# Optimization experiments

Measured on AMD Instinct MI355X. Metric: run time of the kernel, lower is better.

The kernel has to match this reference:

```python
import math
import jax, jax.numpy as jnp
import numpy as np

# config (matches env defaults of the torch module, scaled to production size)
V, D, L, NH, NKV, MLP_M, RECUR, N_VB = 32768, 1024, 6, 16, 8, 3, 2, 5
BG_BK, BG_DIM = 4096, 128
HD = D // NH            # 64 head dim
KV = NKV * HD           # 512 kv width
B, T = 2, 1024
SOFTCAP = 30.0
EPS = 1.1920929e-07     # fp32 eps used by F.rms_norm(eps=None)


def _rms(x):
    return x * jax.lax.rsqrt(jnp.mean(jnp.square(x), axis=-1, keepdims=True) + EPS)


def _rope(x, c, s):
    h = x.shape[-1] // 2
    x1, x2 = x[..., :h], x[..., h:]
    return jnp.concatenate([x1 * c + x2 * s, -x1 * s + x2 * c], axis=-1)


def _forward(ids, tgt, emb, bg_embed, bg_proj, bg_scale, ve,
             Wq, Wk, Wv, Wo, qg, a_s, m_s, mix, Wfc, Wpr):
    Bz, Tz = ids.shape
    # token embedding + bigram-hash embedding
    x = emb[ids]
    t = ids.astype(jnp.int32)
    hv = jnp.bitwise_xor(t[:, 1:] * 36313, t[:, :-1] * 27191) % (BG_BK - 1)
    h = jnp.zeros_like(t).at[:, 1:].set(hv)
    bg = (bg_embed[h] @ bg_proj) * bg_scale
    x = _rms(x + bg)
    x0 = x
    # rope tables
    inv = 1.0 / (10000.0 ** (jnp.arange(0, HD, 2, dtype=jnp.float32) / HD))
    ang = jnp.arange(Tz, dtype=jnp.float32)[:, None] * inv      # (T, HD/2)
    c, s = jnp.cos(ang)[None, None], jnp.sin(ang)[None, None]   # (1,1,T,HD/2)
    mask = jnp.tril(jnp.ones((Tz, Tz), dtype=bool))
    eff = 0
    for _ in range(RECUR):
        for l in range(L):
            vel = ve[eff % N_VB][ids]                            # (B,T,KV)
            m = mix[l]
            x = m[0] * x + m[1] * x0
            # attention
            xn = _rms(x)
            q = (xn @ Wq[l]).reshape(Bz, Tz, NH, HD).transpose(0, 2, 1, 3)
            k = (xn @ Wk[l]).reshape(Bz, Tz, NKV, HD).transpose(0, 2, 1, 3)
            v = ((xn @ Wv[l]) + vel).reshape(Bz, Tz, NKV, HD).transpose(0, 2, 1, 3)
            q, k = _rms(q), _rms(k)
            q, k = _rope(q, c, s), _rope(k, c, s)
            q = q * qg[l][None, :, None, None]
            rep = NH // NKV                                      # GQA expand
            kf = jnp.repeat(k, rep, axis=1)
            vf = jnp.repeat(v, rep, axis=1)
            sc = jnp.einsum('bhqd,bhkd->bhqk', q, kf) / math.sqrt(HD)
            sc = jnp.where(mask, sc, -jnp.inf)
            att = jax.nn.softmax(sc, axis=-1)
            y = jnp.einsum('bhqk,bhkd->bhqd', att, vf)
            y = y.transpose(0, 2, 1, 3).reshape(Bz, Tz, D) @ Wo[l]
            x = x + a_s[l] * y
            # mlp: relu(fc(x))^2 @ proj
            hmid = jnp.square(jax.nn.relu(_rms(x) @ Wfc[l]))
            x = x + m_s[l] * (hmid @ Wpr[l])
            eff += 1
    x = _rms(x)
    lo = x @ emb.T
    lo = SOFTCAP * jnp.tanh(lo / SOFTCAP)
    logp = jax.nn.log_softmax(lo, axis=-1)
    nll = -jnp.take_along_axis(logp, tgt[..., None], axis=-1)[..., 0]
    return jnp.mean(nll)


def setup_inputs() -> dict:
    key = jax.random.key(0)
    ks = jax.random.split(key, 14)
    def nrm(k, shape, std):
        return std * jax.random.normal(k, shape, dtype=jnp.float32)
    eff = L * RECUR
    return {
        'ids': jax.random.randint(ks[0], (B, T), 0, V),
        'tgt': jax.random.randint(ks[1], (B, T), 0, V),
        'emb': nrm(ks[2], (V, D), 0.005),
        'bg_embed': nrm(ks[3], (BG_BK, BG_DIM), 0.02),
        'bg_proj': nrm(ks[4], (BG_DIM, D), 1.0 / math.sqrt(BG_DIM)),
        'bg_scale': jnp.float32(0.05),
        've': nrm(ks[5], (N_VB, V, KV), 0.01),
        'Wq': nrm(ks[6], (L, D, D), 1.0 / math.sqrt(D)),
        'Wk': nrm(ks[7], (L, D, KV), 1.0 / math.sqrt(D)),
        'Wv': nrm(ks[8], (L, D, KV), 1.0 / math.sqrt(D)),
        'Wo': nrm(ks[9], (L, D, D), 1.0 / (math.sqrt(D) * math.sqrt(2 * eff))),
        'qg': jnp.full((L, NH), 1.5, jnp.float32),
        'a_s': jnp.ones((L, D), jnp.float32),
        'm_s': jnp.ones((L, D), jnp.float32),
        'mix': jnp.stack([jnp.ones((L, D)), jnp.zeros((L, D))], axis=1).astype(jnp.float32),
        'Wfc': nrm(ks[10], (L, D, MLP_M * D), 1.0 / math.sqrt(D)),
        'Wpr': nrm(ks[11], (L, MLP_M * D, D), 1.0 / (math.sqrt(MLP_M * D) * math.sqrt(2 * eff))),
    }


def reference(ids, tgt, emb, bg_embed, bg_proj, bg_scale, ve,
              Wq, Wk, Wv, Wo, qg, a_s, m_s, mix, Wfc, Wpr):
    return _forward(ids, tgt, emb, bg_embed, bg_proj, bg_scale, ve,
                    Wq, Wk, Wv, Wo, qg, a_s, m_s, mix, Wfc, Wpr)
```

## Files before the change

### kernel.cpp

```cpp
#include <hip/hip_runtime.h>
#include <hip/hip_bf16.h>
#include <math.h>

#define DEV __device__ __forceinline__

typedef unsigned short u16;
typedef short bf16x8 __attribute__((ext_vector_type(8)));
typedef float f32x4 __attribute__((ext_vector_type(4)));
typedef u16 u16x8 __attribute__((ext_vector_type(8)));
typedef u16 u16x4 __attribute__((ext_vector_type(4)));

#define T_SEQ 1024
#define NTOK 2048
#define DIM 1024
#define NHD 16
#define NKVH 8
#define HDIM 64
#define KVD 512
#define MLPD 3072
#define VOC 32768
#define EPSF 1.1920929e-07f
#define SCAP 30.0f
#define NCB 512
#define PSTRIDE ((size_t)NTOK * DIM)

#define MEMFENCE asm volatile("" ::: "memory")

DEV u16 f2b(float f) {
  __hip_bfloat16 h = __float2bfloat16(f);
  u16 r; __builtin_memcpy(&r, &h, 2); return r;
}
DEV float b2f(u16 u) {
  __hip_bfloat16 h; __builtin_memcpy(&h, &u, 2);
  return __bfloat162float(h);
}

DEV void gload16(const void* g, void* l) {
  __builtin_amdgcn_global_load_lds((const __attribute__((address_space(1))) void*)g,
                                   (__attribute__((address_space(3))) void*)l, 16, 0, 0);
}

DEV float blk_sum256(float v, float* sbuf) {
#pragma unroll
  for (int o = 32; o; o >>= 1) v += __shfl_xor(v, o, 64);
  int w = threadIdx.x >> 6;
  if ((threadIdx.x & 63) == 0) sbuf[w] = v;
  __syncthreads();
  return sbuf[0] + sbuf[1] + sbuf[2] + sbuf[3];
}

__global__ __launch_bounds__(256) void transpose_f2b(const float* __restrict__ in,
    u16* __restrict__ out, int K, int N, size_t in_ls, size_t out_ls) {
  __shared__ float tile[32][33];
  int l = blockIdx.z;
  const float* src = in + (size_t)l * in_ls;
  u16* dst = out + (size_t)l * out_ls;
  int k0 = blockIdx.y << 5, n0 = blockIdx.x << 5;
  int tx = threadIdx.x & 31, ty = threadIdx.x >> 5;
#pragma unroll
  for (int i = 0; i < 32; i += 8)
    tile[ty + i][tx] = src[(size_t)(k0 + ty + i) * N + n0 + tx];
  __syncthreads();
#pragma unroll
  for (int i = 0; i < 32; i += 8)
    dst[(size_t)(n0 + ty + i) * K + k0 + tx] = f2b(tile[tx][ty + i]);
}

__global__ __launch_bounds__(256) void f2b_copy(const float* __restrict__ in,
    u16* __restrict__ out, size_t n) {
  size_t i = ((size_t)blockIdx.x * 256 + threadIdx.x) * 8;
  if (i >= n) return;
  float4 a = *(const float4*)(in + i);
  float4 b = *(const float4*)(in + i + 4);
  u16x8 o;
  o[0] = f2b(a.x); o[1] = f2b(a.y); o[2] = f2b(a.z); o[3] = f2b(a.w);
  o[4] = f2b(b.x); o[5] = f2b(b.y); o[6] = f2b(b.z); o[7] = f2b(b.w);
  *(u16x8*)(out + i) = o;
}

__global__ __launch_bounds__(256) void rope_table(float* __restrict__ rc, float* __restrict__ rs) {
  int idx = blockIdx.x * 256 + threadIdx.x;
  if (idx >= T_SEQ * 32) return;
  int t = idx >> 5, i = idx & 31;
  float inv = expf(-((float)(2 * i) / (float)HDIM) * logf(10000.0f));
  float ang = (float)t * inv;
  rc[idx] = cosf(ang);
  rs[idx] = sinf(ang);
}

__global__ __launch_bounds__(256) void embed_kernel(const int* __restrict__ ids,
    const float* __restrict__ emb, const float* __restrict__ bg_embed,
    const float* __restrict__ bg_proj, const float* __restrict__ bg_scale_p,
    float* __restrict__ x, float* __restrict__ x0) {
  __shared__ float be[128];
  __shared__ float sbuf[4];
  int tok = blockIdx.x, tid = threadIdx.x;
  int t = tok & (T_SEQ - 1);
  int id = ids[tok];
  int hsh = 0;
  if (t > 0) {
    int prev = ids[tok - 1];
    hsh = ((id * 36313) ^ (prev * 27191)) % 4095;
  }
  if (tid < 128) be[tid] = bg_embed[hsh * 128 + tid];
  __syncthreads();
  float scale = bg_scale_p[0];
  const float4* bp = (const float4*)bg_proj;
  float ax = 0.f, ay = 0.f, az = 0.f, aw = 0.f;
#pragma unroll 4
  for (int j = 0; j < 128; ++j) {
    float bj = be[j];
    float4 p = bp[j * 256 + tid];
    ax += bj * p.x; ay += bj * p.y; az += bj * p.z; aw += bj * p.w;
  }
  float4 e = *(const float4*)(emb + (size_t)id * DIM + tid * 4);
  float vx = e.x + ax * scale, vy = e.y + ay * scale;
  float vz = e.z + az * scale, vw = e.w + aw * scale;
  float ss = vx * vx + vy * vy + vz * vz + vw * vw;
  float tot = blk_sum256(ss, sbuf);
  float rn = rsqrtf(tot * (1.0f / DIM) + EPSF);
  float4 o; o.x = vx * rn; o.y = vy * rn; o.z = vz * rn; o.w = vw * rn;
  size_t base = (size_t)tok * DIM + tid * 4;
  *(float4*)(x + base) = o;
  *(float4*)(x0 + base) = o;
}

template <int NP, int MIX>
__global__ __launch_bounds__(256) void norm_k(float* __restrict__ x,
    const float* __restrict__ parts, const float* __restrict__ colscale,
    const float* __restrict__ mixl, const float* __restrict__ x0,
    u16* __restrict__ xn) {
  __shared__ float sbuf[4];
  int tok = blockIdx.x, tid = threadIdx.x;
  size_t base = (size_t)tok * DIM + tid * 4;
  float4 a = *(const float4*)(x + base);
  if (NP > 0) {
    float4 cs = *(const float4*)(colscale + tid * 4);
    float4 s = *(const float4*)(parts + base);
    {
      float4 p = *(const float4*)(parts + PSTRIDE + base);
      s.x += p.x; s.y += p.y; s.z += p.z; s.w += p.w;
    }
    if (NP == 3) {
      float4 p = *(const float4*)(parts + 2 * PSTRIDE + base);
      s.x += p.x; s.y += p.y; s.z += p.z; s.w += p.w;
    }
    a.x += cs.x * s.x; a.y += cs.y * s.y; a.z += cs.z * s.z; a.w += cs.w * s.w;
  }
  if (MIX) {
    float4 m0 = *(const float4*)(mixl + tid * 4);
    float4 m1 = *(const float4*)(mixl + DIM + tid * 4);
    float4 b = *(const float4*)(x0 + base);
    a.x = m0.x * a.x + m1.x * b.x;
    a.y = m0.y * a.y + m1.y * b.y;
    a.z = m0.z * a.z + m1.z * b.z;
    a.w = m0.w * a.w + m1.w * b.w;
  }
  float ss = a.x * a.x + a.y * a.y + a.z * a.z + a.w * a.w;
  float tot = blk_sum256(ss, sbuf);
  float rn = rsqrtf(tot * (1.0f / DIM) + EPSF);
  if (NP > 0 || MIX) *(float4*)(x + base) = a;
  u16x4 q;
  q[0] = f2b(a.x * rn); q[1] = f2b(a.y * rn); q[2] = f2b(a.z * rn); q[3] = f2b(a.w * rn);
  *(u16x4*)(xn + base) = q;
}

template <int EPI, int BN>
__global__ __launch_bounds__(256, (BN == 64 ? 3 : 2)) void gemm_bt(
    const u16* __restrict__ A, const u16* __restrict__ Bt,
    float* __restrict__ Cf, u16* __restrict__ Cb,
    int N, int K, int kpn) {
  constexpr int MF = (BN == 128) ? 4 : 2;
  constexpr int ASZ = 128 * 64;
  constexpr int BSZ = BN * 64;
  constexpr int NLD = 4 + BN / 32;
  __shared__ u16 As[2 * ASZ];
  __shared__ u16 Bs[2 * BSZ];
  int tid = threadIdx.x;
  int wid = tid >> 6, lane = tid & 63;
  int g = lane >> 4, c = lane & 15;
  int row0 = blockIdx.y << 7, col0 = blockIdx.x * BN;
  int kbase = blockIdx.z * kpn;
  int wr = (BN == 128) ? ((wid >> 1) << 6) : (wid << 5);
  int wc = (BN == 128) ? ((wid & 1) << 6) : 0;
  f32x4 acc[MF][4] = {};

  int sr = lane >> 3;
  int kb = lane & 7;
  const u16* srcA[4];
  int ldsA[4];
#pragma unroll
  for (int i = 0; i < 4; ++i) {
    int s = (wid << 2) + i;
    int r = (s << 3) + sr;
    srcA[i] = A + (size_t)(row0 + r) * K + kbase + ((kb ^ (r & 7)) << 3);
    ldsA[i] = s << 9;
  }
  const u16* srcB[BN / 32];
  int ldsB[BN / 32];
#pragma unroll
  for (int i = 0; i < BN / 32; ++i) {
    int s = wid * (BN / 32) + i;
    int r = (s << 3) + sr;
    srcB[i] = Bt + (size_t)(col0 + r) * K + kbase + ((kb ^ (r & 7)) << 3);
    ldsB[i] = s << 9;
  }

#pragma unroll
  for (int i = 0; i < 4; ++i) gload16(srcA[i], As + ldsA[i]);
#pragma unroll
  for (int i = 0; i < BN / 32; ++i) gload16(srcB[i], Bs + ldsB[i]);

  int nk = kpn >> 6;
  for (int t = 0; t < nk; ++t) {
    int cur = t & 1;
    if (t + 1 < nk) {
      int nxt = cur ^ 1;
      int ko = (t + 1) << 6;
#pragma unroll
      for (int i = 0; i < 4; ++i) gload16(srcA[i] + ko, As + nxt * ASZ + ldsA[i]);
#pragma unroll
      for (int i = 0; i < BN / 32; ++i) gload16(srcB[i] + ko, Bs + nxt * BSZ + ldsB[i]);
      if constexpr (NLD == 6) asm volatile("s_waitcnt vmcnt(6)" ::: "memory");
      else asm volatile("s_waitcnt vmcnt(8)" ::: "memory");
    } else {
      asm volatile("s_waitcnt vmcnt(0)" ::: "memory");
    }
    __builtin_amdgcn_s_barrier();
    MEMFENCE;
    const u16* ab = As + cur * ASZ;
    const u16* bb = Bs + cur * BSZ;
#pragma unroll
    for (int ks = 0; ks < 2; ++ks) {
      bf16x8 af[MF], bfr[4];
#pragma unroll
      for (int m = 0; m < MF; ++m) {
        int r = wr + m * 16 + c;
        int kbs = ((ks << 2) + g) ^ (r & 7);
        af[m] = *(const bf16x8*)(ab + r * 64 + (kbs << 3));
      }
#pragma unroll
      for (int n = 0; n < 4; ++n) {
        int r = wc + n * 16 + c;
        int kbs = ((ks << 2) + g) ^ (r & 7);
        bfr[n] = *(const bf16x8*)(bb + r * 64 + (kbs << 3));
      }
      __builtin_amdgcn_s_setprio(1);
#pragma unroll
      for (int m = 0; m < MF; ++m)
#pragma unroll
        for (int n = 0; n < 4; ++n)
          acc[m][n] = __builtin_amdgcn_mfma_f32_16x16x32_bf16(af[m], bfr[n], acc[m][n], 0, 0, 0);
      __builtin_amdgcn_s_setprio(0);
    }
    MEMFENCE;
    __builtin_amdgcn_s_barrier();
  }

  size_t zoff = (size_t)blockIdx.z * PSTRIDE;
#pragma unroll
  for (int m = 0; m < MF; ++m) {
#pragma unroll
    for (int n = 0; n < 4; ++n) {
      int gcol = col0 + wc + n * 16 + c;
#pragma unroll
      for (int j = 0; j < 4; ++j) {
        int grow = row0 + wr + m * 16 + g * 4 + j;
        float v = acc[m][n][j];
        if (EPI == 1) {
          Cf[zoff + (size_t)grow * N + gcol] = v;
        } else if (EPI == 2) {
          float r = v > 0.f ? v : 0.f;
          Cb[(size_t)grow * N + gcol] = f2b(r * r);
        }
      }
    }
  }
}

__global__ __launch_bounds__(512, 2) void gemm_lmhead(
    const u16* __restrict__ A, const u16* __restrict__ Bt,
    const int* __restrict__ tgt, float* __restrict__ pM, float* __restrict__ pS,
    float* __restrict__ loTgt) {
  constexpr int K = 1024;
  constexpr int TSZ = 256 * 64;
  __shared__ u16 As[2 * TSZ];
  __shared__ u16 Bs[2 * TSZ];
  int tid = threadIdx.x;
  int wid = tid >> 6, lane = tid & 63;
  int wm = wid >> 2, wn = wid & 3;
  int g = lane >> 4, c = lane & 15;
  int bid = blockIdx.x;
  int swz = ((bid & 7) << 7) + (bid >> 3);
  int colb = swz >> 3, rowb = swz & 7;
  int row0 = rowb << 8, col0 = colb << 8;
  f32x4 acc[8][4] = {};

  int sr = lane >> 3, kb = lane & 7;
  const u16* srcA[4];
  const u16* srcB[4];
  int ldsOff[4];
#pragma unroll
  for (int i = 0; i < 4; ++i) {
    int s = (wid << 2) + i;
    int r = (s << 3) + sr;
    srcA[i] = A + (size_t)(row0 + r) * K + ((kb ^ (r & 7)) << 3);
    srcB[i] = Bt + (size_t)(col0 + r) * K + ((kb ^ (r & 7)) << 3);
    ldsOff[i] = s << 9;
  }

#pragma unroll
  for (int i = 0; i < 4; ++i) {
    gload16(srcA[i], As + ldsOff[i]);
    gload16(srcB[i], Bs + ldsOff[i]);
  }

  constexpr int nk = K >> 6;
  for (int kt = 0; kt < nk; ++kt) {
    int cur = kt & 1;
    if (kt + 1 < nk) {
      int nxt = cur ^ 1;
      int ko = (kt + 1) << 6;
#pragma unroll
      for (int i = 0; i < 4; ++i) {
        gload16(srcA[i] + ko, As + nxt * TSZ + ldsOff[i]);
        gload16(srcB[i] + ko, Bs + nxt * TSZ + ldsOff[i]);
      }
      asm volatile("s_waitcnt vmcnt(8)" ::: "memory");
    } else {
      asm volatile("s_waitcnt vmcnt(0)" ::: "memory");
    }
    __builtin_amdgcn_s_barrier();
    MEMFENCE;
    const u16* ab = As + cur * TSZ;
    const u16* bb = Bs + cur * TSZ;
    bf16x8 bfr[4][2];
#pragma unroll
    for (int nf = 0; nf < 4; ++nf) {
      int r = (wn << 6) + nf * 16 + c;
#pragma unroll
      for (int ks = 0; ks < 2; ++ks) {
        int kbs = ((ks << 2) + g) ^ (r & 7);
        bfr[nf][ks] = *(const bf16x8*)(bb + r * 64 + (kbs << 3));
      }
    }
#pragma unroll
    for (int p = 0; p < 4; ++p) {
      bf16x8 af[2][2];
#pragma unroll
      for (int mi = 0; mi < 2; ++mi) {
        int r = (wm << 7) + ((p << 1) + mi) * 16 + c;
#pragma unroll
        for (int ks = 0; ks < 2; ++ks) {
          int kbs = ((ks << 2) + g) ^ (r & 7);
          af[mi][ks] = *(const bf16x8*)(ab + r * 64 + (kbs << 3));
        }
      }
      __builtin_amdgcn_s_setprio(1);
#pragma unroll
      for (int ks = 0; ks < 2; ++ks)
#pragma unroll
        for (int mi = 0; mi < 2; ++mi)
#pragma unroll
          for (int nf = 0; nf < 4; ++nf)
            acc[(p << 1) + mi][nf] = __builtin_amdgcn_mfma_f32_16x16x32_bf16(
                af[mi][ks], bfr[nf][ks], acc[(p << 1) + mi][nf], 0, 0, 0);
      __builtin_amdgcn_s_setprio(0);
    }
    MEMFENCE;
    __builtin_amdgcn_s_barrier();
  }

  int cb = (col0 >> 6) + wn;
#pragma unroll
  for (int mf = 0; mf < 8; ++mf) {
#pragma unroll
    for (int j = 0; j < 4; ++j) {
      int grow = row0 + (wm << 7) + mf * 16 + g * 4 + j;
      int tg = tgt[grow];
      float sv[4];
      float mx = -3.0e38f;
#pragma unroll
      for (int nf = 0; nf < 4; ++nf) {
        float a = acc[mf][nf][j] * (1.0f / SCAP);
        a = fminf(fmaxf(a, -15.f), 15.f);
        float e = __expf(2.0f * a);
        float tt = SCAP * (e - 1.0f) / (e + 1.0f);
        sv[nf] = tt;
        mx = fmaxf(mx, tt);
        int gcol = col0 + (wn << 6) + nf * 16 + c;
        if (gcol == tg) loTgt[grow] = tt;
      }
      mx = fmaxf(mx, __shfl_xor(mx, 1, 64));
      mx = fmaxf(mx, __shfl_xor(mx, 2, 64));
      mx = fmaxf(mx, __shfl_xor(mx, 4, 64));
      mx = fmaxf(mx, __shfl_xor(mx, 8, 64));
      float s = 0.f;
#pragma unroll
      for (int nf = 0; nf < 4; ++nf) s += __expf(sv[nf] - mx);
      s += __shfl_xor(s, 1, 64);
      s += __shfl_xor(s, 2, 64);
      s += __shfl_xor(s, 4, 64);
      s += __shfl_xor(s, 8, 64);
      if (c == 0) {
        pM[(size_t)grow * NCB + cb] = mx;
        pS[(size_t)grow * NCB + cb] = s;
      }
    }
  }
}

__global__ __launch_bounds__(256, 3) void gemm_qkv(
    const u16* __restrict__ A, const u16* __restrict__ Bt,
    const float* __restrict__ qg_l, const float* __restrict__ rc, const float* __restrict__ rs,
    const float* __restrict__ ve, const int* __restrict__ ids, int vb,
    u16* __restrict__ qB, u16* __restrict__ kB, u16* __restrict__ vT) {
  constexpr int K = 1024;
  constexpr int ASZ = 128 * 64;
  constexpr int BSZ = 64 * 64;
  __shared__ u16 As[2 * ASZ];
  __shared__ u16 Bs[2 * BSZ];
  int tid = threadIdx.x;
  int wid = tid >> 6, lane = tid & 63;
  int g = lane >> 4, c = lane & 15;
  int bx = blockIdx.x;
  int row0 = blockIdx.y << 7, col0 = bx << 6;
  f32x4 acc[2][4] = {};

  int sr = lane >> 3, kb = lane & 7;
  const u16* srcA[4];
  int ldsA[4];
#pragma unroll
  for (int i = 0; i < 4; ++i) {
    int s = (wid << 2) + i;
    int r = (s << 3) + sr;
    srcA[i] = A + (size_t)(row0 + r) * K + ((kb ^ (r & 7)) << 3);
    ldsA[i] = s << 9;
  }
  const u16* srcB[2];
  int ldsB[2];
#pragma unroll
  for (int i = 0; i < 2; ++i) {
    int s = (wid << 1) + i;
    int r = (s << 3) + sr;
    srcB[i] = Bt + (size_t)(col0 + r) * K + ((kb ^ (r & 7)) << 3);
    ldsB[i] = s << 9;
  }

#pragma unroll
  for (int i = 0; i < 4; ++i) gload16(srcA[i], As + ldsA[i]);
#pragma unroll
  for (int i = 0; i < 2; ++i) gload16(srcB[i], Bs + ldsB[i]);

  for (int t = 0; t < 16; ++t) {
    int cur = t & 1;
    if (t + 1 < 16) {
      int nxt = cur ^ 1;
      int ko = (t + 1) << 6;
#pragma unroll
      for (int i = 0; i < 4; ++i) gload16(srcA[i] + ko, As + nxt * ASZ + ldsA[i]);
#pragma unroll
      for (int i = 0; i < 2; ++i) gload16(srcB[i] + ko, Bs + nxt * BSZ + ldsB[i]);
      asm volatile("s_waitcnt vmcnt(6)" ::: "memory");
    } else {
      asm volatile("s_waitcnt vmcnt(0)" ::: "memory");
    }
    __builtin_amdgcn_s_barrier();
    MEMFENCE;
    const u16* ab = As + cur * ASZ;
    const u16* bb = Bs + cur * BSZ;
#pragma unroll
    for (int ks = 0; ks < 2; ++ks) {
      bf16x8 af[2], bfr[4];
#pragma unroll
      for (int m = 0; m < 2; ++m) {
        int r = (wid << 5) + m * 16 + c;
        int kbs = ((ks << 2) + g) ^ (r & 7);
        af[m] = *(const bf16x8*)(ab + r * 64 + (kbs << 3));
      }
#pragma unroll
      for (int n = 0; n < 4; ++n) {
        int r = n * 16 + c;
        int kbs = ((ks << 2) + g) ^ (r & 7);
        bfr[n] = *(const bf16x8*)(bb + r * 64 + (kbs << 3));
      }
      __builtin_amdgcn_s_setprio(1);
#pragma unroll
      for (int m = 0; m < 2; ++m)
#pragma unroll
        for (int n = 0; n < 4; ++n)
          acc[m][n] = __builtin_amdgcn_mfma_f32_16x16x32_bf16(af[m], bfr[n], acc[m][n], 0, 0, 0);
      __builtin_amdgcn_s_setprio(0);
    }
    MEMFENCE;
    __builtin_amdgcn_s_barrier();
  }

  int b = row0 >> 10;
  if (bx < 24) {
    bool isq = (bx < 16);
    int h = isq ? bx : bx - 16;
    float gmul = isq ? qg_l[h] * 0.125f : 1.0f;
    u16* hb = isq ? (qB + ((size_t)(b * NHD + h)) * T_SEQ * HDIM)
                  : (kB + ((size_t)(b * NKVH + h)) * T_SEQ * HDIM);
#pragma unroll
    for (int m = 0; m < 2; ++m) {
#pragma unroll
      for (int j = 0; j < 4; ++j) {
        int grow = row0 + (wid << 5) + m * 16 + g * 4 + j;
        int t = grow & (T_SEQ - 1);
        float vv[4];
        float ss = 0.f;
#pragma unroll
        for (int n = 0; n < 4; ++n) { vv[n] = acc[m][n][j]; ss += vv[n] * vv[n]; }
        ss += __shfl_xor(ss, 1, 64);
        ss += __shfl_xor(ss, 2, 64);
        ss += __shfl_xor(ss, 4, 64);
        ss += __shfl_xor(ss, 8, 64);
        float rn = rsqrtf(ss * (1.0f / HDIM) + EPSF);
#pragma unroll
        for (int n = 0; n < 4; ++n) vv[n] *= rn;
        float c0 = rc[t * 32 + c], s0 = rs[t * 32 + c];
        float c1 = rc[t * 32 + 16 + c], s1 = rs[t * 32 + 16 + c];
        float o0 = vv[0] * c0 + vv[2] * s0;
        float o1 = vv[1] * c1 + vv[3] * s1;
        float o2 = vv[2] * c0 - vv[0] * s0;
        float o3 = vv[3] * c1 - vv[1] * s1;
        u16* dst = hb + (size_t)t * HDIM;
        dst[c] = f2b(o0 * gmul);
        dst[16 + c] = f2b(o1 * gmul);
        dst[32 + c] = f2b(o2 * gmul);
        dst[48 + c] = f2b(o3 * gmul);
      }
    }
  } else {
    int kh = bx - 24;
#pragma unroll
    for (int m = 0; m < 2; ++m) {
#pragma unroll
      for (int j = 0; j < 4; ++j) {
        int grow = row0 + (wid << 5) + m * 16 + g * 4 + j;
        int lr = (wid << 5) + m * 16 + g * 4 + j;
        int id = ids[grow];
        const float* vl = ve + ((size_t)vb * VOC + id) * KVD + kh * HDIM;
#pragma unroll
        for (int n = 0; n < 4; ++n)
          As[lr * 72 + n * 16 + c] = f2b(acc[m][n][j] + vl[n * 16 + c]);
      }
    }
    __syncthreads();
    int hd = tid & 63, seg = tid >> 6;
    int t0 = (row0 & (T_SEQ - 1)) + seg * 32;
    u16* dst = vT + (((size_t)(b * NKVH + kh)) * HDIM + hd) * T_SEQ + t0;
#pragma unroll
    for (int i = 0; i < 32; i += 8) {
      u16x8 o;
#pragma unroll
      for (int e = 0; e < 8; ++e) o[e] = As[(seg * 32 + i + e) * 72 + hd];
      *(u16x8*)(dst + i) = o;
    }
  }
}

__global__ __launch_bounds__(128) void attn_kernel(const u16* __restrict__ qB,
    const u16* __restrict__ kB, const u16* __restrict__ vT, const float* __restrict__ qg_l,
    u16* __restrict__ attout) {
  __shared__ u16 plds[2][32 * 76];
  int b = blockIdx.z, h = blockIdx.y;
  int kh = h >> 1;
  int wid = threadIdx.x >> 6, lane = threadIdx.x & 63;
  int g = lane >> 4, c = lane & 15;
  int strip = wid ? (31 - (int)blockIdx.x) : (int)blockIdx.x;
  int qr0 = strip << 5;
  const u16* qptr = qB + ((size_t)(b * NHD + h)) * T_SEQ * HDIM;
  const u16* kptr = kB + ((size_t)(b * NKVH + kh)) * T_SEQ * HDIM;
  const u16* vptr = vT + ((size_t)(b * NKVH + kh)) * HDIM * T_SEQ;
  u16* pw = plds[wid];
  float Mh = fabsf(qg_l[h]) * 8.0f;

  bf16x8 aq[2][2];
#pragma unroll
  for (int m = 0; m < 2; ++m)
#pragma unroll
    for (int ks = 0; ks < 2; ++ks)
      aq[m][ks] = *(const bf16x8*)(qptr + (qr0 + m * 16 + c) * HDIM + ks * 32 + g * 8);

  bf16x8 vone;
#pragma unroll
  for (int e = 0; e < 8; ++e) vone[e] = (short)0x3F80;

  f32x4 oacc[2][4] = {};
  f32x4 lacc[2] = {};

  bf16x8 kR0[4][2], vR0[4][2], kR1[4][2], vR1[4][2];

  auto LOADKV = [&](bf16x8 (&bk)[4][2], bf16x8 (&bv)[4][2], int kv0) {
#pragma unroll
    for (int n = 0; n < 4; ++n)
#pragma unroll
      for (int ks = 0; ks < 2; ++ks) {
        bk[n][ks] = *(const bf16x8*)(kptr + (kv0 + n * 16 + c) * HDIM + ks * 32 + g * 8);
        bv[n][ks] = *(const bf16x8*)(vptr + (n * 16 + c) * T_SEQ + kv0 + ks * 32 + g * 8);
      }
  };

  auto BODY = [&](bf16x8 (&bk)[4][2], bf16x8 (&bv)[4][2], int kv0) {
    f32x4 sc[2][4] = {};
#pragma unroll
    for (int ks = 0; ks < 2; ++ks)
#pragma unroll
      for (int m = 0; m < 2; ++m)
#pragma unroll
        for (int n = 0; n < 4; ++n)
          sc[m][n] = __builtin_amdgcn_mfma_f32_16x16x32_bf16(aq[m][ks], bk[n][ks], sc[m][n], 0, 0, 0);
    bool maskT = (kv0 + 64 > qr0);
#pragma unroll
    for (int m = 0; m < 2; ++m) {
#pragma unroll
      for (int j = 0; j < 4; ++j) {
        int row = qr0 + m * 16 + g * 4 + j;
        float p0 = __expf(sc[m][0][j] - Mh);
        float p1 = __expf(sc[m][1][j] - Mh);
        float p2 = __expf(sc[m][2][j] - Mh);
        float p3 = __expf(sc[m][3][j] - Mh);
        if (maskT) {
          if (kv0 + c > row) p0 = 0.f;
          if (kv0 + 16 + c > row) p1 = 0.f;
          if (kv0 + 32 + c > row) p2 = 0.f;
          if (kv0 + 48 + c > row) p3 = 0.f;
        }
        int pr = m * 16 + g * 4 + j;
        pw[pr * 76 + c] = f2b(p0);
        pw[pr * 76 + 16 + c] = f2b(p1);
        pw[pr * 76 + 32 + c] = f2b(p2);
        pw[pr * 76 + 48 + c] = f2b(p3);
      }
    }
    MEMFENCE;
    bf16x8 ap[2][2];
#pragma unroll
    for (int m = 0; m < 2; ++m)
#pragma unroll
      for (int ks = 0; ks < 2; ++ks) {
        u16x8 tmp = *(const u16x8*)(pw + (m * 16 + c) * 76 + ks * 32 + g * 8);
        __builtin_memcpy(&ap[m][ks], &tmp, 16);
      }
#pragma unroll
    for (int ks = 0; ks < 2; ++ks) {
#pragma unroll
      for (int m = 0; m < 2; ++m) {
#pragma unroll
        for (int n = 0; n < 4; ++n)
          oacc[m][n] = __builtin_amdgcn_mfma_f32_16x16x32_bf16(ap[m][ks], bv[n][ks], oacc[m][n], 0, 0, 0);
        lacc[m] = __builtin_amdgcn_mfma_f32_16x16x32_bf16(ap[m][ks], vone, lacc[m], 0, 0, 0);
      }
    }
  };

  LOADKV(kR0, vR0, 0);
  int kv0 = 0;
  while (true) {
    if (kv0 + 64 <= qr0) LOADKV(kR1, vR1, kv0 + 64);
    BODY(kR0, vR0, kv0);
    kv0 += 64;
    if (kv0 > qr0) break;
    if (kv0 + 64 <= qr0) LOADKV(kR0, vR0, kv0 + 64);
    BODY(kR1, vR1, kv0);
    kv0 += 64;
    if (kv0 > qr0) break;
  }

#pragma unroll
  for (int m = 0; m < 2; ++m) {
#pragma unroll
    for (int j = 0; j < 4; ++j) {
      float inv = 1.0f / lacc[m][j];
      int trow = qr0 + m * 16 + g * 4 + j;
      u16* orow = attout + ((size_t)(b * T_SEQ + trow)) * DIM + h * HDIM;
#pragma unroll
      for (int n = 0; n < 4; ++n)
        orow[n * 16 + c] = f2b(oacc[m][n][j] * inv);
    }
  }
}

__global__ __launch_bounds__(256) void lse_merge(const float* __restrict__ pM,
    const float* __restrict__ pS, const float* __restrict__ loTgt, float* __restrict__ nll) {
  __shared__ float sbuf[4];
  int tok = blockIdx.x, tid = threadIdx.x;
  int wid = tid >> 6, lane = tid & 63;
  const float* rm = pM + (size_t)tok * NCB;
  const float* rs = pS + (size_t)tok * NCB;
  float m0 = rm[tid], m1 = rm[tid + 256];
  float mx = fmaxf(m0, m1);
#pragma unroll
  for (int o = 32; o; o >>= 1) mx = fmaxf(mx, __shfl_xor(mx, o, 64));
  if (lane == 0) sbuf[wid] = mx;
  __syncthreads();
  float M = fmaxf(fmaxf(sbuf[0], sbuf[1]), fmaxf(sbuf[2], sbuf[3]));
  __syncthreads();
  float s = rs[tid] * __expf(m0 - M) + rs[tid + 256] * __expf(m1 - M);
  float S = blk_sum256(s, sbuf);
  if (tid == 0) nll[tok] = logf(S) + M - loTgt[tok];
}

__global__ __launch_bounds__(256) void loss_final(const float* __restrict__ nll,
    float* __restrict__ out) {
  __shared__ float sbuf[4];
  int tid = threadIdx.x;
  float acc = 0.f;
  for (int i = tid; i < NTOK; i += 256) acc += nll[i];
  float tot = blk_sum256(acc, sbuf);
  if (tid == 0) out[0] = tot * (1.0f / NTOK);
}

extern "C" void kernel_launch(void* const* d_in, const int* in_sizes, int n_in,
                              void* d_out, int out_size, void* d_ws, size_t ws_size,
                              hipStream_t stream) {
  (void)in_sizes; (void)n_in; (void)out_size; (void)ws_size;
  const int* ids = (const int*)d_in[0];
  const int* tgt = (const int*)d_in[1];
  const float* emb = (const float*)d_in[2];
  const float* bg_embed = (const float*)d_in[3];
  const float* bg_proj = (const float*)d_in[4];
  const float* bg_scale = (const float*)d_in[5];
  const float* ve = (const float*)d_in[6];
  const float* Wq = (const float*)d_in[7];
  const float* Wk = (const float*)d_in[8];
  const float* Wv = (const float*)d_in[9];
  const float* Wo = (const float*)d_in[10];
  const float* qg = (const float*)d_in[11];
  const float* a_s = (const float*)d_in[12];
  const float* m_s = (const float*)d_in[13];
  const float* mix = (const float*)d_in[14];
  const float* Wfc = (const float*)d_in[15];
  const float* Wpr = (const float*)d_in[16];

  char* w = (char*)d_ws;
  auto alloc = [&](size_t bytes) {
    char* p = w;
    w += (bytes + 255) & ~(size_t)255;
    return p;
  };
  u16* WqkvT = (u16*)alloc(6ull * 2048 * 1024 * 2);
  u16* WoT   = (u16*)alloc(6ull * 1024 * 1024 * 2);
  u16* WfcT  = (u16*)alloc(6ull * 3072 * 1024 * 2);
  u16* WprT  = (u16*)alloc(6ull * 1024 * 3072 * 2);
  u16* embB  = (u16*)alloc((size_t)VOC * DIM * 2);
  float* x   = (float*)alloc((size_t)NTOK * DIM * 4);
  float* x0  = (float*)alloc((size_t)NTOK * DIM * 4);
  u16* xn    = (u16*)alloc((size_t)NTOK * DIM * 2);
  u16* qBuf  = (u16*)alloc((size_t)NTOK * DIM * 2);
  u16* kBuf  = (u16*)alloc((size_t)NTOK * KVD * 2);
  u16* vTb   = (u16*)alloc((size_t)NTOK * KVD * 2);
  u16* attout = (u16*)alloc((size_t)NTOK * DIM * 2);
  u16* xmlp  = (u16*)alloc((size_t)NTOK * DIM * 2);
  u16* hmid  = (u16*)alloc((size_t)NTOK * MLPD * 2);
  float* pparts = (float*)alloc(3 * PSTRIDE * 4);
  float* rc  = (float*)alloc((size_t)T_SEQ * 32 * 4);
  float* rs  = (float*)alloc((size_t)T_SEQ * 32 * 4);
  float* pM  = (float*)alloc((size_t)NTOK * NCB * 4);
  float* pS  = (float*)alloc((size_t)NTOK * NCB * 4);
  float* loTgt = (float*)alloc(NTOK * 4);
  float* nll = (float*)alloc(NTOK * 4);

  transpose_f2b<<<dim3(32, 32, 6), 256, 0, stream>>>(Wq, WqkvT, 1024, 1024,
      (size_t)1024 * 1024, (size_t)2048 * 1024);
  transpose_f2b<<<dim3(16, 32, 6), 256, 0, stream>>>(Wk, WqkvT + 1024 * 1024, 1024, 512,
      (size_t)1024 * 512, (size_t)2048 * 1024);
  transpose_f2b<<<dim3(16, 32, 6), 256, 0, stream>>>(Wv, WqkvT + 1536 * 1024, 1024, 512,
      (size_t)1024 * 512, (size_t)2048 * 1024);
  transpose_f2b<<<dim3(32, 32, 6), 256, 0, stream>>>(Wo, WoT, 1024, 1024,
      (size_t)1024 * 1024, (size_t)1024 * 1024);
  transpose_f2b<<<dim3(96, 32, 6), 256, 0, stream>>>(Wfc, WfcT, 1024, 3072,
      (size_t)1024 * 3072, (size_t)3072 * 1024);
  transpose_f2b<<<dim3(32, 96, 6), 256, 0, stream>>>(Wpr, WprT, 3072, 1024,
      (size_t)3072 * 1024, (size_t)1024 * 3072);
  f2b_copy<<<16384, 256, 0, stream>>>(emb, embB, (size_t)VOC * DIM);
  rope_table<<<128, 256, 0, stream>>>(rc, rs);
  embed_kernel<<<NTOK, 256, 0, stream>>>(ids, emb, bg_embed, bg_proj, bg_scale, x, x0);

  int lprev = 0;
  for (int step = 0; step < 12; ++step) {
    int l = step % 6;
    if (step == 0)
      norm_k<0, 1><<<NTOK, 256, 0, stream>>>(x, nullptr, nullptr, mix + l * 2048, x0, xn);
    else
      norm_k<3, 1><<<NTOK, 256, 0, stream>>>(x, pparts, m_s + lprev * DIM, mix + l * 2048, x0, xn);
    gemm_qkv<<<dim3(32, 16), 256, 0, stream>>>(xn, WqkvT + (size_t)l * 2048 * 1024,
        qg + l * 16, rc, rs, ve, ids, step % 5, qBuf, kBuf, vTb);
    attn_kernel<<<dim3(16, 16, 2), 128, 0, stream>>>(qBuf, kBuf, vTb, qg + l * 16, attout);
    gemm_bt<1, 64><<<dim3(16, 16, 2), 256, 0, stream>>>(attout, WoT + (size_t)l * 1024 * 1024,
        pparts, nullptr, 1024, 1024, 512);
    norm_k<2, 0><<<NTOK, 256, 0, stream>>>(x, pparts, a_s + l * DIM, nullptr, nullptr, xmlp);
    gemm_bt<2, 64><<<dim3(48, 16, 1), 256, 0, stream>>>(xmlp, WfcT + (size_t)l * 3072 * 1024,
        nullptr, hmid, 3072, 1024, 1024);
    gemm_bt<1, 64><<<dim3(16, 16, 3), 256, 0, stream>>>(hmid, WprT + (size_t)l * 1024 * 3072,
        pparts, nullptr, 1024, 3072, 1024);
    lprev = l;
  }

  norm_k<3, 0><<<NTOK, 256, 0, stream>>>(x, pparts, m_s + lprev * DIM, nullptr, nullptr, xn);
  gemm_lmhead<<<1024, 512, 0, stream>>>(xn, embB, tgt, pM, pS, loTgt);
  lse_merge<<<NTOK, 256, 0, stream>>>(pM, pS, loTgt, nll);
  loss_final<<<1, 256, 0, stream>>>(nll, (float*)d_out);
}
```

Before: 1.868 ms.

## Split attention KV range across two blocks and merge partials; fuse prep kernels

Attention is split along the KV dimension: each block handles every other 64-wide KV tile. The two blocks write unnormalized fp32 partial outputs and row sums, and a new merge kernel adds them and normalizes into bf16. This doubles the attention grid to fill more compute units, since the old grid had only 512 blocks of 128 threads. In exchange it adds an fp32 round trip through global memory and one extra launch per layer. The weight-transpose, embedding-conversion and rope-table setup kernels are also merged into one launch to cut launch overhead.

```diff
diff --git a/kernel.cpp b/kernel.cpp
--- a/kernel.cpp
+++ b/kernel.cpp
@@ -49,43 +49,56 @@
   return sbuf[0] + sbuf[1] + sbuf[2] + sbuf[3];
 }
 
-__global__ __launch_bounds__(256) void transpose_f2b(const float* __restrict__ in,
-    u16* __restrict__ out, int K, int N, size_t in_ls, size_t out_ls) {
-  __shared__ float tile[32][33];
-  int l = blockIdx.z;
-  const float* src = in + (size_t)l * in_ls;
-  u16* dst = out + (size_t)l * out_ls;
-  int k0 = blockIdx.y << 5, n0 = blockIdx.x << 5;
-  int tx = threadIdx.x & 31, ty = threadIdx.x >> 5;
-#pragma unroll
-  for (int i = 0; i < 32; i += 8)
-    tile[ty + i][tx] = src[(size_t)(k0 + ty + i) * N + n0 + tx];
-  __syncthreads();
-#pragma unroll
-  for (int i = 0; i < 32; i += 8)
-    dst[(size_t)(n0 + ty + i) * K + k0 + tx] = f2b(tile[tx][ty + i]);
-}
-
-__global__ __launch_bounds__(256) void f2b_copy(const float* __restrict__ in,
-    u16* __restrict__ out, size_t n) {
-  size_t i = ((size_t)blockIdx.x * 256 + threadIdx.x) * 8;
-  if (i >= n) return;
-  float4 a = *(const float4*)(in + i);
-  float4 b = *(const float4*)(in + i + 4);
-  u16x8 o;
-  o[0] = f2b(a.x); o[1] = f2b(a.y); o[2] = f2b(a.z); o[3] = f2b(a.w);
-  o[4] = f2b(b.x); o[5] = f2b(b.y); o[6] = f2b(b.z); o[7] = f2b(b.w);
-  *(u16x8*)(out + i) = o;
-}
-
-__global__ __launch_bounds__(256) void rope_table(float* __restrict__ rc, float* __restrict__ rs) {
-  int idx = blockIdx.x * 256 + threadIdx.x;
-  if (idx >= T_SEQ * 32) return;
-  int t = idx >> 5, i = idx & 31;
-  float inv = expf(-((float)(2 * i) / (float)HDIM) * logf(10000.0f));
-  float ang = (float)t * inv;
-  rc[idx] = cosf(ang);
-  rs[idx] = sinf(ang);
+__global__ __launch_bounds__(256) void prep_all(
+    const float* __restrict__ Wq, const float* __restrict__ Wk, const float* __restrict__ Wv,
+    const float* __restrict__ Wo, const float* __restrict__ Wfc, const float* __restrict__ Wpr,
+    const float* __restrict__ emb,
+    u16* __restrict__ WqkvT, u16* __restrict__ WoT, u16* __restrict__ WfcT,
+    u16* __restrict__ WprT, u16* __restrict__ embB,
+    float* __restrict__ rc, float* __restrict__ rs) {
+  int bid = blockIdx.x;
+  if (bid < 55296) {
+    const float* in; u16* out; int nx, K, N; size_t in_ls, out_ls; int base;
+    if (bid < 6144)       { base = 0;     in = Wq;  out = WqkvT;           nx = 32; K = 1024; N = 1024; in_ls = 1048576; out_ls = 2097152; }
+    else if (bid < 9216)  { base = 6144;  in = Wk;  out = WqkvT + 1048576; nx = 16; K = 1024; N = 512;  in_ls = 524288;  out_ls = 2097152; }
+    else if (bid < 12288) { base = 9216;  in = Wv;  out = WqkvT + 1572864; nx = 16; K = 1024; N = 512;  in_ls = 524288;  out_ls = 2097152; }
+    else if (bid < 18432) { base = 12288; in = Wo;  out = WoT;             nx = 32; K = 1024; N = 1024; in_ls = 1048576; out_ls = 1048576; }
+    else if (bid < 36864) { base = 18432; in = Wfc; out = WfcT;            nx = 96; K = 1024; N = 3072; in_ls = 3145728; out_ls = 3145728; }
+    else                  { base = 36864; in = Wpr; out = WprT;            nx = 32; K = 3072; N = 1024; in_ls = 3145728; out_ls = 3145728; }
+    int local = bid - base;
+    int kx = local % nx;
+    int rest = local / nx;
+    int ny = K >> 5;
+    int ky = rest % ny;
+    int l = rest / ny;
+    __shared__ float tile[32][33];
+    const float* src = in + (size_t)l * in_ls;
+    u16* dst = out + (size_t)l * out_ls;
+    int k0 = ky << 5, n0 = kx << 5;
+    int tx = threadIdx.x & 31, ty = threadIdx.x >> 5;
+#pragma unroll
+    for (int i = 0; i < 32; i += 8)
+      tile[ty + i][tx] = src[(size_t)(k0 + ty + i) * N + n0 + tx];
+    __syncthreads();
+#pragma unroll
+    for (int i = 0; i < 32; i += 8)
+      dst[(size_t)(n0 + ty + i) * K + k0 + tx] = f2b(tile[tx][ty + i]);
+  } else if (bid < 71680) {
+    size_t i = ((size_t)(bid - 55296) * 256 + threadIdx.x) * 8;
+    float4 a = *(const float4*)(emb + i);
+    float4 b = *(const float4*)(emb + i + 4);
+    u16x8 o;
+    o[0] = f2b(a.x); o[1] = f2b(a.y); o[2] = f2b(a.z); o[3] = f2b(a.w);
+    o[4] = f2b(b.x); o[5] = f2b(b.y); o[6] = f2b(b.z); o[7] = f2b(b.w);
+    *(u16x8*)(embB + i) = o;
+  } else {
+    int idx = (bid - 71680) * 256 + threadIdx.x;
+    int t = idx >> 5, i2 = idx & 31;
+    float inv = expf(-((float)(2 * i2) / (float)HDIM) * logf(10000.0f));
+    float ang = (float)t * inv;
+    rc[idx] = cosf(ang);
+    rs[idx] = sinf(ang);
+  }
 }
 
 __global__ __launch_bounds__(256) void embed_kernel(const int* __restrict__ ids,
@@ -564,9 +577,11 @@
 
 __global__ __launch_bounds__(128) void attn_kernel(const u16* __restrict__ qB,
     const u16* __restrict__ kB, const u16* __restrict__ vT, const float* __restrict__ qg_l,
-    u16* __restrict__ attout) {
+    float* __restrict__ oPart, float* __restrict__ lPart) {
   __shared__ u16 plds[2][32 * 76];
-  int b = blockIdx.z, h = blockIdx.y;
+  int z = blockIdx.z;
+  int b = z & 1, half = z >> 1;
+  int h = blockIdx.y;
   int kh = h >> 1;
   int wid = threadIdx.x >> 6, lane = threadIdx.x & 63;
   int g = lane >> 4, c = lane & 15;
@@ -657,31 +672,55 @@
     }
   };
 
-  LOADKV(kR0, vR0, 0);
-  int kv0 = 0;
-  while (true) {
-    if (kv0 + 64 <= qr0) LOADKV(kR1, vR1, kv0 + 64);
-    BODY(kR0, vR0, kv0);
-    kv0 += 64;
-    if (kv0 > qr0) break;
-    if (kv0 + 64 <= qr0) LOADKV(kR0, vR0, kv0 + 64);
-    BODY(kR1, vR1, kv0);
-    kv0 += 64;
-    if (kv0 > qr0) break;
-  }
-
+  int kv0 = half << 6;
+  if (kv0 <= qr0) {
+    LOADKV(kR0, vR0, kv0);
+    while (true) {
+      int nxt = kv0 + 128;
+      if (nxt <= qr0) LOADKV(kR1, vR1, nxt);
+      BODY(kR0, vR0, kv0);
+      kv0 = nxt;
+      if (kv0 > qr0) break;
+      nxt = kv0 + 128;
+      if (nxt <= qr0) LOADKV(kR0, vR0, nxt);
+      BODY(kR1, vR1, kv0);
+      kv0 = nxt;
+      if (kv0 > qr0) break;
+    }
+  }
+
+  size_t pbase = (size_t)((half * 2 + b) * NHD + h) * T_SEQ;
 #pragma unroll
   for (int m = 0; m < 2; ++m) {
 #pragma unroll
     for (int j = 0; j < 4; ++j) {
-      float inv = 1.0f / lacc[m][j];
       int trow = qr0 + m * 16 + g * 4 + j;
-      u16* orow = attout + ((size_t)(b * T_SEQ + trow)) * DIM + h * HDIM;
+      float* orow = oPart + (pbase + trow) * HDIM;
 #pragma unroll
       for (int n = 0; n < 4; ++n)
-        orow[n * 16 + c] = f2b(oacc[m][n][j] * inv);
-    }
-  }
+        orow[n * 16 + c] = oacc[m][n][j];
+      if (c == 0) lPart[pbase + trow] = lacc[m][j];
+    }
+  }
+}
+
+__global__ __launch_bounds__(256) void attn_merge(const float* __restrict__ oPart,
+    const float* __restrict__ lPart, u16* __restrict__ attout) {
+  int tok = blockIdx.x;
+  int b = tok >> 10, t = tok & (T_SEQ - 1);
+  int col = threadIdx.x << 2;
+  int h = col >> 6, d = col & 63;
+  size_t i0 = (size_t)((0 * 2 + b) * NHD + h) * T_SEQ + t;
+  size_t i1 = (size_t)((1 * 2 + b) * NHD + h) * T_SEQ + t;
+  float4 o0 = *(const float4*)(oPart + i0 * HDIM + d);
+  float4 o1 = *(const float4*)(oPart + i1 * HDIM + d);
+  float inv = 1.0f / (lPart[i0] + lPart[i1]);
+  u16x4 q;
+  q[0] = f2b((o0.x + o1.x) * inv);
+  q[1] = f2b((o0.y + o1.y) * inv);
+  q[2] = f2b((o0.z + o1.z) * inv);
+  q[3] = f2b((o0.w + o1.w) * inv);
+  *(u16x4*)(attout + (size_t)tok * DIM + col) = q;
 }
 
 __global__ __launch_bounds__(256) void lse_merge(const float* __restrict__ pM,
@@ -763,21 +802,11 @@
   float* pS  = (float*)alloc((size_t)NTOK * NCB * 4);
   float* loTgt = (float*)alloc(NTOK * 4);
   float* nll = (float*)alloc(NTOK * 4);
-
-  transpose_f2b<<<dim3(32, 32, 6), 256, 0, stream>>>(Wq, WqkvT, 1024, 1024,
-      (size_t)1024 * 1024, (size_t)2048 * 1024);
-  transpose_f2b<<<dim3(16, 32, 6), 256, 0, stream>>>(Wk, WqkvT + 1024 * 1024, 1024, 512,
-      (size_t)1024 * 512, (size_t)2048 * 1024);
-  transpose_f2b<<<dim3(16, 32, 6), 256, 0, stream>>>(Wv, WqkvT + 1536 * 1024, 1024, 512,
-      (size_t)1024 * 512, (size_t)2048 * 1024);
-  transpose_f2b<<<dim3(32, 32, 6), 256, 0, stream>>>(Wo, WoT, 1024, 1024,
-      (size_t)1024 * 1024, (size_t)1024 * 1024);
-  transpose_f2b<<<dim3(96, 32, 6), 256, 0, stream>>>(Wfc, WfcT, 1024, 3072,
-      (size_t)1024 * 3072, (size_t)3072 * 1024);
-  transpose_f2b<<<dim3(32, 96, 6), 256, 0, stream>>>(Wpr, WprT, 3072, 1024,
-      (size_t)3072 * 1024, (size_t)1024 * 3072);
-  f2b_copy<<<16384, 256, 0, stream>>>(emb, embB, (size_t)VOC * DIM);
-  rope_table<<<128, 256, 0, stream>>>(rc, rs);
+  float* oPart = (float*)alloc(4ull * NHD * T_SEQ * HDIM * 4);
+  float* lPart = (float*)alloc(4ull * NHD * T_SEQ * 4);
+
+  prep_all<<<71808, 256, 0, stream>>>(Wq, Wk, Wv, Wo, Wfc, Wpr, emb,
+      WqkvT, WoT, WfcT, WprT, embB, rc, rs);
   embed_kernel<<<NTOK, 256, 0, stream>>>(ids, emb, bg_embed, bg_proj, bg_scale, x, x0);
 
   int lprev = 0;
@@ -789,7 +818,9 @@
       norm_k<3, 1><<<NTOK, 256, 0, stream>>>(x, pparts, m_s + lprev * DIM, mix + l * 2048, x0, xn);
     gemm_qkv<<<dim3(32, 16), 256, 0, stream>>>(xn, WqkvT + (size_t)l * 2048 * 1024,
         qg + l * 16, rc, rs, ve, ids, step % 5, qBuf, kBuf, vTb);
-    attn_kernel<<<dim3(16, 16, 2), 128, 0, stream>>>(qBuf, kBuf, vTb, qg + l * 16, attout);
+    attn_kernel<<<dim3(16, 16, 4), 128, 0, stream>>>(qBuf, kBuf, vTb, qg + l * 16,
+        oPart, lPart);
+    attn_merge<<<NTOK, 256, 0, stream>>>(oPart, lPart, attout);
     gemm_bt<1, 64><<<dim3(16, 16, 2), 256, 0, stream>>>(attout, WoT + (size_t)l * 1024 * 1024,
         pparts, nullptr, 1024, 1024, 512);
     norm_k<2, 0><<<NTOK, 256, 0, stream>>>(x, pparts, a_s + l * DIM, nullptr, nullptr, xmlp);
```

Result: slower. 1.942 ms (+3.9%).
